# Kernel optimization log

Hardware: AMD Instinct MI355X
Metric: run time of the kernel (lower is better)

The kernel has to match this reference:

```python
import jax, jax.numpy as jnp
import numpy as np

B, T, IN, H, OUT = 4096, 7, 512, 1024, 512


def setup_inputs() -> dict:
    key = jax.random.key(0)
    ks = jax.random.split(key, 13)
    s = 0.05  # weight init scale to keep gates/tanh unsaturated
    return {
        "x": jax.random.normal(ks[0], (B, T, IN), jnp.float32),
        "W_ih1": jax.random.normal(ks[1], (3 * H, IN), jnp.float32) * s,
        "W_hh1": jax.random.normal(ks[2], (3 * H, H), jnp.float32) * s,
        "b_ih1": jax.random.normal(ks[3], (3 * H,), jnp.float32) * s,
        "b_hh1": jax.random.normal(ks[4], (3 * H,), jnp.float32) * s,
        "W_ih2": jax.random.normal(ks[5], (3 * H, H), jnp.float32) * s,
        "W_hh2": jax.random.normal(ks[6], (3 * H, H), jnp.float32) * s,
        "b_ih2": jax.random.normal(ks[7], (3 * H,), jnp.float32) * s,
        "b_hh2": jax.random.normal(ks[8], (3 * H,), jnp.float32) * s,
        "Wo1": jax.random.normal(ks[9], (OUT, H), jnp.float32) * s,
        "bo1": jax.random.normal(ks[10], (OUT,), jnp.float32) * s,
        "Wo2": jax.random.normal(ks[11], (OUT, H), jnp.float32) * s,
        "bo2": jax.random.normal(ks[12], (OUT,), jnp.float32) * s,
    }


def gru_cell(x, h, W_ih, W_hh, b_ih, b_hh):
    # torch.nn.GRUCell math, gate order (r, z, n)
    gi = x @ W_ih.T + b_ih          # [B, 3H]
    gh = h @ W_hh.T + b_hh          # [B, 3H]
    i_r, i_z, i_n = jnp.split(gi, 3, axis=-1)
    h_r, h_z, h_n = jnp.split(gh, 3, axis=-1)
    r = jax.nn.sigmoid(i_r + h_r)
    z = jax.nn.sigmoid(i_z + h_z)
    n = jnp.tanh(i_n + r * h_n)
    return (1.0 - z) * n + z * h


def reference(x, W_ih1, W_hh1, b_ih1, b_hh1, W_ih2, W_hh2, b_ih2, b_hh2,
              Wo1, bo1, Wo2, bo2):
    batch = x.shape[0]
    h1_0 = jnp.zeros((batch, H), x.dtype)
    h2_0 = jnp.zeros((batch, H), x.dtype)

    def step(carry, x_t):
        h1, h2 = carry
        h1 = gru_cell(x_t, h1, W_ih1, W_hh1, b_ih1, b_hh1)
        h2 = gru_cell(h1, h2, W_ih2, W_hh2, b_ih2, b_hh2)
        out = jnp.tanh(h1 @ Wo1.T + bo1) + jnp.tanh(h2 @ Wo2.T + bo2)
        # s_t_cached starts as T zeros and only T steps run, so the popped
        # cached state is always zeros: mse(h2, 0) == mean(h2**2)
        aux = jnp.mean(jnp.square(h2))
        return (h1, h2), (out, aux)

    xs = jnp.swapaxes(x, 0, 1)  # [T, B, IN]
    _, (outs, auxs) = jax.lax.scan(step, (h1_0, h2_0), xs)
    outputs = jnp.swapaxes(outs, 0, 1)  # [B, T, OUT]
    aux_loss = jnp.sum(auxs)
    return outputs, aux_loss
```

## Files before the change

### kernel.cpp

```cpp
#include <hip/hip_runtime.h>
#include <cstdint>

#define BB   4096
#define TT   7
#define INF  512
#define HH   1024
#define OUTF 512
#define G3   3072

typedef short bf16x8 __attribute__((ext_vector_type(8)));
typedef float f32x4  __attribute__((ext_vector_type(4)));

static __device__ __forceinline__ unsigned short f2bf(float f) {
  unsigned u = __float_as_uint(f);
  unsigned r = ((u >> 16) & 1u) + 0x7FFFu;
  return (unsigned short)((u + r) >> 16);
}
static __device__ __forceinline__ float bf2f(unsigned short s) {
  return __uint_as_float(((unsigned)s) << 16);
}

#define GLDS16(gp, lp)                                                        \
  __builtin_amdgcn_global_load_lds(                                           \
      (const __attribute__((address_space(1))) void*)(gp),                    \
      (__attribute__((address_space(3))) void*)(lp), 16, 0, 0)

__device__ __forceinline__ int xcd_swz(int bid, int nwg) {
  return (bid & 7) * (nwg >> 3) + (bid >> 3);
}

__global__ __launch_bounds__(256)
void cvt_f32_to_bf16_x4(const float* __restrict__ in, unsigned short* __restrict__ out, int n4) {
  int i = blockIdx.x * 256 + threadIdx.x;
  if (i >= n4) return;
  const float4 v = ((const float4*)in)[i];
  ushort4 o;
  o.x = f2bf(v.x); o.y = f2bf(v.y); o.z = f2bf(v.z); o.w = f2bf(v.w);
  ((ushort4*)out)[i] = o;
}

template<int BM, int BN, int WM, int WN, int GN>
__device__ __forceinline__ void gemm_core(
    const unsigned short* __restrict__ A, long lda, long bm,
    const unsigned short* __restrict__ Wp, long ldw, int K,
    const float* __restrict__ biasp,
    void* __restrict__ Cp, long ldc,
    const float* __restrict__ addp, long ldadd, int mode)
{
  constexpr int ABUF = BM * 64;
  constexpr int WBUF = BN * 64;
  constexpr int AR = (BM * 8) / 256;
  constexpr int WR = (BN * 8) / 256;
  __shared__ __attribute__((aligned(16))) unsigned short sm[2 * (ABUF + WBUF)];
  unsigned short* As = sm;
  unsigned short* Ws = sm + 2 * ABUF;
  __attribute__((address_space(3))) unsigned short* lAs =
      (__attribute__((address_space(3))) unsigned short*)As;
  __attribute__((address_space(3))) unsigned short* lWs =
      (__attribute__((address_space(3))) unsigned short*)Ws;

  const int tid  = threadIdx.x;
  const int lane = tid & 63;
  const int wid  = tid >> 6;
  const int wr = (wid / GN) * (WM * 16);
  const int wc = (wid % GN) * (WN * 16);
  const int fr = lane & 15;
  const int q2 = lane >> 4;

  const unsigned short* gpa[AR];
  const unsigned short* gpw[WR];
  int lofa[AR], lofw[WR];
#pragma unroll
  for (int r = 0; r < AR; ++r) {
    const int id = r * 256 + tid;
    const int row = id >> 3, cc = id & 7;
    gpa[r] = A + (bm + row) * lda + (cc ^ (row & 7)) * 8;
    lofa[r] = id * 8;
  }
#pragma unroll
  for (int r = 0; r < WR; ++r) {
    const int id = r * 256 + tid;
    const int row = id >> 3, cc = id & 7;
    gpw[r] = Wp + (long)row * ldw + (cc ^ (row & 7)) * 8;
    lofw[r] = id * 8;
  }

#define STAGE(buf, kt) do {                                                   \
    _Pragma("unroll")                                                         \
    for (int r = 0; r < AR; ++r) GLDS16(gpa[r] + (kt), lAs + (buf) * ABUF + lofa[r]); \
    _Pragma("unroll")                                                         \
    for (int r = 0; r < WR; ++r) GLDS16(gpw[r] + (kt), lWs + (buf) * WBUF + lofw[r]); \
  } while (0)

  f32x4 acc[WM][WN] = {};
  STAGE(0, 0);
  __syncthreads();
  const int NK = K >> 6;
  for (int it = 0; it < NK; ++it) {
    const int cur = it & 1;
    if (it + 1 < NK) STAGE(cur ^ 1, (it + 1) << 6);

#pragma unroll
    for (int ks = 0; ks < 2; ++ks) {
      bf16x8 af[WM], wf[WN];
#pragma unroll
      for (int i = 0; i < WM; ++i) {
        const int row = wr + i * 16 + fr;
        const int ch  = (ks * 4 + q2) ^ (row & 7);
        af[i] = *(const bf16x8*)&As[cur * ABUF + row * 64 + ch * 8];
      }
#pragma unroll
      for (int i = 0; i < WN; ++i) {
        const int row = wc + i * 16 + fr;
        const int ch  = (ks * 4 + q2) ^ (row & 7);
        wf[i] = *(const bf16x8*)&Ws[cur * WBUF + row * 64 + ch * 8];
      }
#pragma unroll
      for (int mi = 0; mi < WM; ++mi)
#pragma unroll
        for (int ni = 0; ni < WN; ++ni)
          acc[mi][ni] = __builtin_amdgcn_mfma_f32_16x16x32_bf16(af[mi], wf[ni], acc[mi][ni], 0, 0, 0);
    }
    __syncthreads();
  }
#undef STAGE

  const int q = lane >> 4;
#pragma unroll
  for (int ni = 0; ni < WN; ++ni) {
    const int col = wc + ni * 16 + fr;
    const float bv = biasp[col];
#pragma unroll
    for (int mi = 0; mi < WM; ++mi) {
      const long row = bm + wr + mi * 16 + q * 4;
#pragma unroll
      for (int j = 0; j < 4; ++j) {
        const float v = acc[mi][ni][j] + bv;
        if (mode == 0)      ((float*)Cp)[(row + j) * ldc + col] = v;
        else if (mode == 1) ((float*)Cp)[(row + j) * ldc + col] = tanhf(v);
        else if (mode == 2) ((float*)Cp)[(row + j) * ldc + col] = tanhf(v) + addp[(row + j) * ldadd + col];
        else                ((unsigned short*)Cp)[(row + j) * ldc + col] = f2bf(v);
      }
    }
  }
}

__global__ __launch_bounds__(256)
void k_gi1(const unsigned short* __restrict__ A, long lda,
           const unsigned short* __restrict__ W, const float* __restrict__ bias,
           unsigned short* __restrict__ C, int gx)
{
  const int wg = xcd_swz(blockIdx.x, gridDim.x);
  const int bx = wg % gx, by = wg / gx;
  gemm_core<128,128,4,4,2>(A, lda, (long)bx * 128, W + (long)by * 128 * INF, INF, INF,
                           bias + by * 128, C + by * 128, G3, nullptr, 0, 3);
}

__global__ __launch_bounds__(256)
void k_gh_dual(const unsigned short* __restrict__ h1b, const unsigned short* __restrict__ h2b,
               const unsigned short* __restrict__ W1, const unsigned short* __restrict__ W2,
               const float* __restrict__ b1, const float* __restrict__ b2,
               unsigned short* __restrict__ gh1, unsigned short* __restrict__ gh2)
{
  const int wg = xcd_swz(blockIdx.x, gridDim.x);
  const int bx = wg % 32;
  const int by = (wg / 32) % 24;
  const int z  = wg / (32 * 24);
  const unsigned short* Aa = z ? h2b : h1b;
  const unsigned short* Ww = (z ? W2 : W1) + (long)by * 128 * HH;
  const float* bias = (z ? b2 : b1) + by * 128;
  unsigned short* C = (z ? gh2 : gh1) + by * 128;
  gemm_core<128,128,4,4,2>(Aa, HH, (long)bx * 128, Ww, HH, HH, bias, C, G3, nullptr, 0, 3);
}

__global__ __launch_bounds__(256)
void k_gi2_o1(const unsigned short* __restrict__ h1b,
              const unsigned short* __restrict__ Wih2, const float* __restrict__ bih2,
              unsigned short* __restrict__ gi2,
              const unsigned short* __restrict__ Wo1, const float* __restrict__ bo1,
              float* __restrict__ o1t)
{
  const int wg = xcd_swz(blockIdx.x, gridDim.x);
  const int bx = wg % 32;
  const int by = wg / 32;
  const bool g = (by < 24);
  const int bo = by - 24;
  const unsigned short* Ww = g ? (Wih2 + (long)by * 128 * HH) : (Wo1 + (long)bo * 128 * HH);
  const float* bias        = g ? (bih2 + by * 128)            : (bo1 + bo * 128);
  void* C                  = g ? (void*)(gi2 + by * 128)      : (void*)(o1t + bo * 128);
  const long ldc           = g ? (long)G3 : (long)OUTF;
  gemm_core<128,128,4,4,2>(h1b, HH, (long)bx * 128, Ww, HH, HH, bias, C, ldc,
                           nullptr, 0, g ? 3 : 1);
}

__global__ __launch_bounds__(256)
void k_o2_out(const unsigned short* __restrict__ h2b,
              const unsigned short* __restrict__ Wo2, const float* __restrict__ bo2,
              const float* __restrict__ o1t, float* __restrict__ outp)
{
  const int wg = xcd_swz(blockIdx.x, gridDim.x);
  const int bx = wg % 64;
  const int by = wg / 64;
  gemm_core<64,64,2,2,2>(h2b, HH, (long)bx * 64, Wo2 + (long)by * 64 * HH, HH, HH,
                         bo2 + by * 64, outp + by * 64, (long)TT * OUTF,
                         o1t + by * 64, OUTF, 2);
}

__global__ __launch_bounds__(256)
void k_gate(const unsigned short* __restrict__ gi, long gistride,
            const unsigned short* __restrict__ gh,
            unsigned short* __restrict__ hb,
            float* __restrict__ auxp)
{
  const int i4 = blockIdx.x * 256 + threadIdx.x;
  const int e  = i4 << 2;
  const int b = e >> 10;
  const int c = e & 1023;
  const unsigned short* g = gi + (long)b * gistride + c;
  const ushort4 a0 = *(const ushort4*)(g);
  const ushort4 a1 = *(const ushort4*)(g + HH);
  const ushort4 a2 = *(const ushort4*)(g + 2 * HH);
  const unsigned short* gg = gh + (long)b * G3 + c;
  const ushort4 b0 = *(const ushort4*)(gg);
  const ushort4 b1 = *(const ushort4*)(gg + HH);
  const ushort4 b2 = *(const ushort4*)(gg + 2 * HH);
  const f32x4 ir  = f32x4{bf2f(a0.x), bf2f(a0.y), bf2f(a0.z), bf2f(a0.w)};
  const f32x4 iz  = f32x4{bf2f(a1.x), bf2f(a1.y), bf2f(a1.z), bf2f(a1.w)};
  const f32x4 inn = f32x4{bf2f(a2.x), bf2f(a2.y), bf2f(a2.z), bf2f(a2.w)};
  const f32x4 hr  = f32x4{bf2f(b0.x), bf2f(b0.y), bf2f(b0.z), bf2f(b0.w)};
  const f32x4 hz  = f32x4{bf2f(b1.x), bf2f(b1.y), bf2f(b1.z), bf2f(b1.w)};
  const f32x4 hn  = f32x4{bf2f(b2.x), bf2f(b2.y), bf2f(b2.z), bf2f(b2.w)};
  const ushort4 ho = *(const ushort4*)(hb + e);
  const f32x4 h = f32x4{bf2f(ho.x), bf2f(ho.y), bf2f(ho.z), bf2f(ho.w)};
  f32x4 hnew;
  float vsum = 0.f;
#pragma unroll
  for (int j = 0; j < 4; ++j) {
    const float r = 1.f / (1.f + __expf(-(ir[j] + hr[j])));
    const float z = 1.f / (1.f + __expf(-(iz[j] + hz[j])));
    const float n = tanhf(inn[j] + r * hn[j]);
    hnew[j] = (1.f - z) * n + z * h[j];
    vsum += hnew[j] * hnew[j];
  }
  ushort4 o;
  o.x = f2bf(hnew[0]); o.y = f2bf(hnew[1]); o.z = f2bf(hnew[2]); o.w = f2bf(hnew[3]);
  *(ushort4*)(hb + e) = o;
  if (auxp != nullptr) {
#pragma unroll
    for (int off = 32; off > 0; off >>= 1) vsum += __shfl_down(vsum, off);
    __shared__ float wsum[4];
    if ((threadIdx.x & 63) == 0) wsum[threadIdx.x >> 6] = vsum;
    __syncthreads();
    if (threadIdx.x == 0) auxp[blockIdx.x] = wsum[0] + wsum[1] + wsum[2] + wsum[3];
  }
}

__global__ __launch_bounds__(256)
void aux_reduce(const float* __restrict__ p, int n, float* __restrict__ out, float scale) {
  float s = 0.f;
  for (int i = threadIdx.x; i < n; i += 256) s += p[i];
#pragma unroll
  for (int off = 32; off > 0; off >>= 1) s += __shfl_down(s, off);
  __shared__ float wsum[4];
  if ((threadIdx.x & 63) == 0) wsum[threadIdx.x >> 6] = s;
  __syncthreads();
  if (threadIdx.x == 0) out[0] = (wsum[0] + wsum[1] + wsum[2] + wsum[3]) * scale;
}

extern "C" void kernel_launch(void* const* d_in, const int* in_sizes, int n_in,
                              void* d_out, int out_size, void* d_ws, size_t ws_size,
                              hipStream_t stream) {
  const float* x    = (const float*)d_in[0];
  const float* Wih1 = (const float*)d_in[1];
  const float* Whh1 = (const float*)d_in[2];
  const float* bih1 = (const float*)d_in[3];
  const float* bhh1 = (const float*)d_in[4];
  const float* Wih2 = (const float*)d_in[5];
  const float* Whh2 = (const float*)d_in[6];
  const float* bih2 = (const float*)d_in[7];
  const float* bhh2 = (const float*)d_in[8];
  const float* Wo1  = (const float*)d_in[9];
  const float* bo1  = (const float*)d_in[10];
  const float* Wo2  = (const float*)d_in[11];
  const float* bo2  = (const float*)d_in[12];

  char* ws = (char*)d_ws;
  size_t off = 0;
  auto alloc = [&](size_t bytes) {
    char* p = ws + off;
    off = (off + bytes + 255) & ~(size_t)255;
    return p;
  };

  unsigned short* xb    = (unsigned short*)alloc((size_t)BB * TT * INF * 2);
  unsigned short* wih1b = (unsigned short*)alloc((size_t)G3 * INF * 2);
  unsigned short* whh1b = (unsigned short*)alloc((size_t)G3 * HH * 2);
  unsigned short* wih2b = (unsigned short*)alloc((size_t)G3 * HH * 2);
  unsigned short* whh2b = (unsigned short*)alloc((size_t)G3 * HH * 2);
  unsigned short* wo1b  = (unsigned short*)alloc((size_t)OUTF * HH * 2);
  unsigned short* wo2b  = (unsigned short*)alloc((size_t)OUTF * HH * 2);
  unsigned short* h1b = (unsigned short*)alloc((size_t)BB * HH * 2);
  unsigned short* h2b = (unsigned short*)alloc((size_t)BB * HH * 2);
  unsigned short* gh1 = (unsigned short*)alloc((size_t)BB * G3 * 2);
  unsigned short* gh2 = (unsigned short*)alloc((size_t)BB * G3 * 2);
  float* o1t  = (float*)alloc((size_t)BB * OUTF * 4);
  float* auxp = (float*)alloc((size_t)TT * (BB * HH / 1024) * 4);
  unsigned short* gi2 = gh1;

  const size_t gi1_big   = (size_t)BB * TT * G3 * 2;
  const size_t gi1_small = (size_t)BB * G3 * 2;
  const bool hoist = (off + gi1_big + (size_t)(32 << 20)) <= ws_size;
  unsigned short* gi1b = (unsigned short*)alloc(hoist ? gi1_big : gi1_small);

  float* aux = (float*)d_out + (size_t)BB * TT * OUTF;

  auto cvt = [&](const float* src, unsigned short* dst, size_t n) {
    int n4 = (int)(n / 4);
    cvt_f32_to_bf16_x4<<<dim3((n4 + 255) / 256), dim3(256), 0, stream>>>(src, dst, n4);
  };
  cvt(x,    xb,    (size_t)BB * TT * INF);
  cvt(Wih1, wih1b, (size_t)G3 * INF);
  cvt(Whh1, whh1b, (size_t)G3 * HH);
  cvt(Wih2, wih2b, (size_t)G3 * HH);
  cvt(Whh2, whh2b, (size_t)G3 * HH);
  cvt(Wo1,  wo1b,  (size_t)OUTF * HH);
  cvt(Wo2,  wo2b,  (size_t)OUTF * HH);

  hipMemsetAsync(h1b, 0, (size_t)BB * HH * 2, stream);
  hipMemsetAsync(h2b, 0, (size_t)BB * HH * 2, stream);

  const dim3 blk(256);
  const int gateGrid = BB * HH / 1024;

  if (hoist)
    k_gi1<<<dim3(224 * 24), blk, 0, stream>>>(xb, INF, wih1b, bih1, gi1b, 224);

  for (int t = 0; t < TT; ++t) {
    if (!hoist)
      k_gi1<<<dim3(32 * 24), blk, 0, stream>>>(xb + (size_t)t * INF, (long)TT * INF,
                                               wih1b, bih1, gi1b, 32);
    k_gh_dual<<<dim3(32 * 24 * 2), blk, 0, stream>>>(h1b, h2b, whh1b, whh2b, bhh1, bhh2, gh1, gh2);
    k_gate<<<dim3(gateGrid), blk, 0, stream>>>(
        hoist ? gi1b + (size_t)t * G3 : gi1b, hoist ? (long)TT * G3 : (long)G3,
        gh1, h1b, nullptr);
    k_gi2_o1<<<dim3(32 * 28), blk, 0, stream>>>(h1b, wih2b, bih2, gi2, wo1b, bo1, o1t);
    k_gate<<<dim3(gateGrid), blk, 0, stream>>>(gi2, (long)G3, gh2, h2b,
                                               auxp + (size_t)t * gateGrid);
    k_o2_out<<<dim3(64 * 8), blk, 0, stream>>>(h2b, wo2b, bo2, o1t,
                                               (float*)d_out + (size_t)t * OUTF);
  }
  aux_reduce<<<dim3(1), blk, 0, stream>>>(auxp, TT * gateGrid, aux,
                                          1.f / ((float)BB * (float)HH));
}
```

Measured before the change: 1.416 ms.

## Merge per-step gi1, gh and delayed o2 GEMMs into one launch; single-buffer K=32 tiles

Merges the per-timestep x-projection GEMM, both recurrent hidden GEMMs and the previous step's output-2 GEMM into one grid. This cuts launches and fills the GPU with more workgroups per wave. The hoisted all-timestep input GEMM is dropped in favour of per-step computation. The GEMM core also moves from double-buffered 64-wide K tiles with XOR swizzle to single-buffered 32-wide tiles with no swizzle, halving LDS use. That may raise occupancy, but it adds two barriers per iteration, exposes load latency and risks LDS bank conflicts.

```diff
diff --git a/kernel.cpp b/kernel.cpp
--- a/kernel.cpp
+++ b/kernel.cpp
@@ -47,13 +47,11 @@
     void* __restrict__ Cp, long ldc,
     const float* __restrict__ addp, long ldadd, int mode)
 {
-  constexpr int ABUF = BM * 64;
-  constexpr int WBUF = BN * 64;
-  constexpr int AR = (BM * 8) / 256;
-  constexpr int WR = (BN * 8) / 256;
-  __shared__ __attribute__((aligned(16))) unsigned short sm[2 * (ABUF + WBUF)];
+  constexpr int AR = (BM * 4) / 256;
+  constexpr int WR = (BN * 4) / 256;
+  __shared__ __attribute__((aligned(16))) unsigned short sm[(BM + BN) * 32];
   unsigned short* As = sm;
-  unsigned short* Ws = sm + 2 * ABUF;
+  unsigned short* Ws = sm + BM * 32;
   __attribute__((address_space(3))) unsigned short* lAs =
       (__attribute__((address_space(3))) unsigned short*)As;
   __attribute__((address_space(3))) unsigned short* lWs =
@@ -65,7 +63,7 @@
   const int wr = (wid / GN) * (WM * 16);
   const int wc = (wid % GN) * (WN * 16);
   const int fr = lane & 15;
-  const int q2 = lane >> 4;
+  const int fk = (lane >> 4) * 8;
 
   const unsigned short* gpa[AR];
   const unsigned short* gpw[WR];
@@ -73,57 +71,38 @@
 #pragma unroll
   for (int r = 0; r < AR; ++r) {
     const int id = r * 256 + tid;
-    const int row = id >> 3, cc = id & 7;
-    gpa[r] = A + (bm + row) * lda + (cc ^ (row & 7)) * 8;
+    gpa[r] = A + (bm + (id >> 2)) * lda + (id & 3) * 8;
     lofa[r] = id * 8;
   }
 #pragma unroll
   for (int r = 0; r < WR; ++r) {
     const int id = r * 256 + tid;
-    const int row = id >> 3, cc = id & 7;
-    gpw[r] = Wp + (long)row * ldw + (cc ^ (row & 7)) * 8;
+    gpw[r] = Wp + (long)(id >> 2) * ldw + (id & 3) * 8;
     lofw[r] = id * 8;
   }
 
-#define STAGE(buf, kt) do {                                                   \
-    _Pragma("unroll")                                                         \
-    for (int r = 0; r < AR; ++r) GLDS16(gpa[r] + (kt), lAs + (buf) * ABUF + lofa[r]); \
-    _Pragma("unroll")                                                         \
-    for (int r = 0; r < WR; ++r) GLDS16(gpw[r] + (kt), lWs + (buf) * WBUF + lofw[r]); \
-  } while (0)
-
   f32x4 acc[WM][WN] = {};
-  STAGE(0, 0);
-  __syncthreads();
-  const int NK = K >> 6;
-  for (int it = 0; it < NK; ++it) {
-    const int cur = it & 1;
-    if (it + 1 < NK) STAGE(cur ^ 1, (it + 1) << 6);
-
-#pragma unroll
-    for (int ks = 0; ks < 2; ++ks) {
-      bf16x8 af[WM], wf[WN];
-#pragma unroll
-      for (int i = 0; i < WM; ++i) {
-        const int row = wr + i * 16 + fr;
-        const int ch  = (ks * 4 + q2) ^ (row & 7);
-        af[i] = *(const bf16x8*)&As[cur * ABUF + row * 64 + ch * 8];
-      }
-#pragma unroll
-      for (int i = 0; i < WN; ++i) {
-        const int row = wc + i * 16 + fr;
-        const int ch  = (ks * 4 + q2) ^ (row & 7);
-        wf[i] = *(const bf16x8*)&Ws[cur * WBUF + row * 64 + ch * 8];
-      }
-#pragma unroll
-      for (int mi = 0; mi < WM; ++mi)
-#pragma unroll
-        for (int ni = 0; ni < WN; ++ni)
-          acc[mi][ni] = __builtin_amdgcn_mfma_f32_16x16x32_bf16(af[mi], wf[ni], acc[mi][ni], 0, 0, 0);
-    }
+  for (int kt = 0; kt < K; kt += 32) {
+    if (kt) __syncthreads();
+#pragma unroll
+    for (int r = 0; r < AR; ++r) GLDS16(gpa[r] + kt, lAs + lofa[r]);
+#pragma unroll
+    for (int r = 0; r < WR; ++r) GLDS16(gpw[r] + kt, lWs + lofw[r]);
     __syncthreads();
-  }
-#undef STAGE
+
+    bf16x8 af[WM], wf[WN];
+#pragma unroll
+    for (int i = 0; i < WM; ++i)
+      af[i] = *(const bf16x8*)&As[(wr + i * 16 + fr) * 32 + fk];
+#pragma unroll
+    for (int i = 0; i < WN; ++i)
+      wf[i] = *(const bf16x8*)&Ws[(wc + i * 16 + fr) * 32 + fk];
+#pragma unroll
+    for (int mi = 0; mi < WM; ++mi)
+#pragma unroll
+      for (int ni = 0; ni < WN; ++ni)
+        acc[mi][ni] = __builtin_amdgcn_mfma_f32_16x16x32_bf16(af[mi], wf[ni], acc[mi][ni], 0, 0, 0);
+  }
 
   const int q = lane >> 4;
 #pragma unroll
@@ -146,31 +125,45 @@
 }
 
 __global__ __launch_bounds__(256)
-void k_gi1(const unsigned short* __restrict__ A, long lda,
-           const unsigned short* __restrict__ W, const float* __restrict__ bias,
-           unsigned short* __restrict__ C, int gx)
+void k_step1(const unsigned short* __restrict__ xb_t,
+             const unsigned short* __restrict__ wih1b, const float* __restrict__ bih1,
+             unsigned short* __restrict__ gi1b,
+             const unsigned short* __restrict__ h1b, const unsigned short* __restrict__ h2b,
+             const unsigned short* __restrict__ whh1b, const unsigned short* __restrict__ whh2b,
+             const float* __restrict__ bhh1, const float* __restrict__ bhh2,
+             unsigned short* __restrict__ gh1, unsigned short* __restrict__ gh2,
+             const unsigned short* __restrict__ wo2b, const float* __restrict__ bo2,
+             const float* __restrict__ o1t_prev, float* __restrict__ out_prev)
 {
   const int wg = xcd_swz(blockIdx.x, gridDim.x);
-  const int bx = wg % gx, by = wg / gx;
-  gemm_core<128,128,4,4,2>(A, lda, (long)bx * 128, W + (long)by * 128 * INF, INF, INF,
-                           bias + by * 128, C + by * 128, G3, nullptr, 0, 3);
-}
-
-__global__ __launch_bounds__(256)
-void k_gh_dual(const unsigned short* __restrict__ h1b, const unsigned short* __restrict__ h2b,
-               const unsigned short* __restrict__ W1, const unsigned short* __restrict__ W2,
-               const float* __restrict__ b1, const float* __restrict__ b2,
-               unsigned short* __restrict__ gh1, unsigned short* __restrict__ gh2)
-{
-  const int wg = xcd_swz(blockIdx.x, gridDim.x);
-  const int bx = wg % 32;
-  const int by = (wg / 32) % 24;
-  const int z  = wg / (32 * 24);
-  const unsigned short* Aa = z ? h2b : h1b;
-  const unsigned short* Ww = (z ? W2 : W1) + (long)by * 128 * HH;
-  const float* bias = (z ? b2 : b1) + by * 128;
-  unsigned short* C = (z ? gh2 : gh1) + by * 128;
-  gemm_core<128,128,4,4,2>(Aa, HH, (long)bx * 128, Ww, HH, HH, bias, C, G3, nullptr, 0, 3);
+  const unsigned short* A; long lda; long bm;
+  const unsigned short* W; long ldw; int K;
+  const float* bias; void* C; long ldc; int mode;
+  const float* addp = nullptr; long ldadd = 0;
+  if (wg < 768) {
+    const int bx = wg & 31, by = wg >> 5;
+    A = xb_t; lda = (long)TT * INF; bm = (long)bx * 128;
+    W = wih1b + (long)by * 128 * INF; ldw = INF; K = INF;
+    bias = bih1 + by * 128; C = gi1b + by * 128; ldc = G3; mode = 3;
+  } else if (wg < 2304) {
+    int idx = wg - 768;
+    const int z = idx >= 768;
+    if (z) idx -= 768;
+    const int bx = idx & 31, by = idx >> 5;
+    A = z ? h2b : h1b; lda = HH; bm = (long)bx * 128;
+    W = (z ? whh2b : whh1b) + (long)by * 128 * HH; ldw = HH; K = HH;
+    bias = (z ? bhh2 : bhh1) + by * 128;
+    C = (z ? gh2 : gh1) + by * 128; ldc = G3; mode = 3;
+  } else {
+    const int idx = wg - 2304;
+    const int bx = idx & 31, by = idx >> 5;
+    A = h2b; lda = HH; bm = (long)bx * 128;
+    W = wo2b + (long)by * 128 * HH; ldw = HH; K = HH;
+    bias = bo2 + by * 128;
+    C = out_prev + by * 128; ldc = (long)TT * OUTF; mode = 2;
+    addp = o1t_prev + by * 128; ldadd = OUTF;
+  }
+  gemm_core<128,128,4,4,2>(A, lda, bm, W, ldw, K, bias, C, ldc, addp, ldadd, mode);
 }
 
 __global__ __launch_bounds__(256)
@@ -181,8 +174,8 @@
               float* __restrict__ o1t)
 {
   const int wg = xcd_swz(blockIdx.x, gridDim.x);
-  const int bx = wg % 32;
-  const int by = wg / 32;
+  const int bx = wg & 31;
+  const int by = wg >> 5;
   const bool g = (by < 24);
   const int bo = by - 24;
   const unsigned short* Ww = g ? (Wih2 + (long)by * 128 * HH) : (Wo1 + (long)bo * 128 * HH);
@@ -194,16 +187,16 @@
 }
 
 __global__ __launch_bounds__(256)
-void k_o2_out(const unsigned short* __restrict__ h2b,
-              const unsigned short* __restrict__ Wo2, const float* __restrict__ bo2,
-              const float* __restrict__ o1t, float* __restrict__ outp)
+void k_o2f(const unsigned short* __restrict__ h2b,
+           const unsigned short* __restrict__ Wo2, const float* __restrict__ bo2,
+           const float* __restrict__ o1t, float* __restrict__ outp)
 {
   const int wg = xcd_swz(blockIdx.x, gridDim.x);
-  const int bx = wg % 64;
-  const int by = wg / 64;
-  gemm_core<64,64,2,2,2>(h2b, HH, (long)bx * 64, Wo2 + (long)by * 64 * HH, HH, HH,
-                         bo2 + by * 64, outp + by * 64, (long)TT * OUTF,
-                         o1t + by * 64, OUTF, 2);
+  const int bx = wg & 31;
+  const int by = wg >> 5;
+  gemm_core<128,128,4,4,2>(h2b, HH, (long)bx * 128, Wo2 + (long)by * 128 * HH, HH, HH,
+                           bo2 + by * 128, outp + by * 128, (long)TT * OUTF,
+                           o1t + by * 128, OUTF, 2);
 }
 
 __global__ __launch_bounds__(256)
@@ -303,14 +296,10 @@
   unsigned short* h2b = (unsigned short*)alloc((size_t)BB * HH * 2);
   unsigned short* gh1 = (unsigned short*)alloc((size_t)BB * G3 * 2);
   unsigned short* gh2 = (unsigned short*)alloc((size_t)BB * G3 * 2);
+  unsigned short* gi1b = (unsigned short*)alloc((size_t)BB * G3 * 2);
   float* o1t  = (float*)alloc((size_t)BB * OUTF * 4);
   float* auxp = (float*)alloc((size_t)TT * (BB * HH / 1024) * 4);
   unsigned short* gi2 = gh1;
-
-  const size_t gi1_big   = (size_t)BB * TT * G3 * 2;
-  const size_t gi1_small = (size_t)BB * G3 * 2;
-  const bool hoist = (off + gi1_big + (size_t)(32 << 20)) <= ws_size;
-  unsigned short* gi1b = (unsigned short*)alloc(hoist ? gi1_big : gi1_small);
 
   float* aux = (float*)d_out + (size_t)BB * TT * OUTF;
 
@@ -332,23 +321,19 @@
   const dim3 blk(256);
   const int gateGrid = BB * HH / 1024;
 
-  if (hoist)
-    k_gi1<<<dim3(224 * 24), blk, 0, stream>>>(xb, INF, wih1b, bih1, gi1b, 224);
-
   for (int t = 0; t < TT; ++t) {
-    if (!hoist)
-      k_gi1<<<dim3(32 * 24), blk, 0, stream>>>(xb + (size_t)t * INF, (long)TT * INF,
-                                               wih1b, bih1, gi1b, 32);
-    k_gh_dual<<<dim3(32 * 24 * 2), blk, 0, stream>>>(h1b, h2b, whh1b, whh2b, bhh1, bhh2, gh1, gh2);
-    k_gate<<<dim3(gateGrid), blk, 0, stream>>>(
-        hoist ? gi1b + (size_t)t * G3 : gi1b, hoist ? (long)TT * G3 : (long)G3,
-        gh1, h1b, nullptr);
+    const int d1grid = (t == 0) ? 2304 : 2432;
+    k_step1<<<dim3(d1grid), blk, 0, stream>>>(
+        xb + (size_t)t * INF, wih1b, bih1, gi1b,
+        h1b, h2b, whh1b, whh2b, bhh1, bhh2, gh1, gh2,
+        wo2b, bo2, o1t, (float*)d_out + (size_t)(t > 0 ? t - 1 : 0) * OUTF);
+    k_gate<<<dim3(gateGrid), blk, 0, stream>>>(gi1b, (long)G3, gh1, h1b, nullptr);
     k_gi2_o1<<<dim3(32 * 28), blk, 0, stream>>>(h1b, wih2b, bih2, gi2, wo1b, bo1, o1t);
     k_gate<<<dim3(gateGrid), blk, 0, stream>>>(gi2, (long)G3, gh2, h2b,
                                                auxp + (size_t)t * gateGrid);
-    k_o2_out<<<dim3(64 * 8), blk, 0, stream>>>(h2b, wo2b, bo2, o1t,
-                                               (float*)d_out + (size_t)t * OUTF);
-  }
+  }
+  k_o2f<<<dim3(128), blk, 0, stream>>>(h2b, wo2b, bo2, o1t,
+                                       (float*)d_out + (size_t)(TT - 1) * OUTF);
   aux_reduce<<<dim3(1), blk, 0, stream>>>(auxp, TT * gateGrid, aux,
                                           1.f / ((float)BB * (float)HH));
 }
```

Result: slower. 1.881 ms (+32.8%).

## Use 256x256 tile GEMM with 512-thread blocks and per-step input projection

Applied to the files above, without the earlier changes.

Adds a 256x256-tile GEMM core with 8 waves, each computing 128x64 of the tile, and uses it for the input-projection, hidden-projection and gi2/o1 kernels. This cuts grid sizes to a few hundred workgroups and raises operand reuse per LDS load. The hoisted all-timestep input projection is dropped, so gi1 is now computed each step into a small buffer. The goal is better MFMA density and less LDS and global traffic, at the cost of 128KB of LDS per block, fewer blocks (limited wave-level parallelism), and more register pressure.

```diff
diff --git a/kernel.cpp b/kernel.cpp
--- a/kernel.cpp
+++ b/kernel.cpp
@@ -37,6 +37,122 @@
   ushort4 o;
   o.x = f2bf(v.x); o.y = f2bf(v.y); o.z = f2bf(v.z); o.w = f2bf(v.w);
   ((ushort4*)out)[i] = o;
+}
+
+__device__ __forceinline__ void gemm256_core(
+    const unsigned short* __restrict__ A, long lda, long bm,
+    const unsigned short* __restrict__ Wp, long ldw, int K,
+    const float* __restrict__ biasp,
+    void* __restrict__ Cp, long ldc,
+    const float* __restrict__ addp, long ldadd, int mode)
+{
+  constexpr int TBUF = 256 * 64;
+  __shared__ __attribute__((aligned(16))) unsigned short sm[4 * TBUF];
+  unsigned short* As = sm;
+  unsigned short* Ws = sm + 2 * TBUF;
+  __attribute__((address_space(3))) unsigned short* lAs =
+      (__attribute__((address_space(3))) unsigned short*)As;
+  __attribute__((address_space(3))) unsigned short* lWs =
+      (__attribute__((address_space(3))) unsigned short*)Ws;
+
+  const int tid  = threadIdx.x;
+  const int lane = tid & 63;
+  const int wid  = tid >> 6;
+  const int wr = (wid >> 2) * 128;
+  const int wc = (wid & 3) * 64;
+  const int fr = lane & 15;
+  const int q2 = lane >> 4;
+
+  const unsigned short* gpa[4];
+  const unsigned short* gpw[4];
+  int lof[4];
+#pragma unroll
+  for (int r = 0; r < 4; ++r) {
+    const int id = r * 512 + tid;
+    const int row = id >> 3, cc = id & 7;
+    gpa[r] = A + (bm + row) * lda + (cc ^ (row & 7)) * 8;
+    gpw[r] = Wp + (long)row * ldw + (cc ^ (row & 7)) * 8;
+    lof[r] = id * 8;
+  }
+
+#define STAGE256(buf, kt) do {                                                \
+    _Pragma("unroll")                                                         \
+    for (int r = 0; r < 4; ++r) GLDS16(gpa[r] + (kt), lAs + (buf) * TBUF + lof[r]); \
+    _Pragma("unroll")                                                         \
+    for (int r = 0; r < 4; ++r) GLDS16(gpw[r] + (kt), lWs + (buf) * TBUF + lof[r]); \
+  } while (0)
+
+  f32x4 acc[8][4] = {};
+  STAGE256(0, 0);
+  __syncthreads();
+  const int NT = K >> 6;
+  for (int it = 0; it < NT; ++it) {
+    const int cur = it & 1;
+    if (it + 1 < NT) STAGE256(cur ^ 1, (it + 1) << 6);
+
+    bf16x8 bfr[4][2];
+#pragma unroll
+    for (int ni = 0; ni < 4; ++ni)
+#pragma unroll
+      for (int ks = 0; ks < 2; ++ks) {
+        const int row = wc + ni * 16 + fr;
+        const int ch  = (ks * 4 + q2) ^ (row & 7);
+        bfr[ni][ks] = *(const bf16x8*)&Ws[cur * TBUF + row * 64 + ch * 8];
+      }
+    {
+      bf16x8 af[8];
+#pragma unroll
+      for (int mi = 0; mi < 8; ++mi) {
+        const int row = wr + mi * 16 + fr;
+        const int ch  = q2 ^ (row & 7);
+        af[mi] = *(const bf16x8*)&As[cur * TBUF + row * 64 + ch * 8];
+      }
+      __builtin_amdgcn_s_setprio(1);
+#pragma unroll
+      for (int mi = 0; mi < 8; ++mi)
+#pragma unroll
+        for (int ni = 0; ni < 4; ++ni)
+          acc[mi][ni] = __builtin_amdgcn_mfma_f32_16x16x32_bf16(af[mi], bfr[ni][0], acc[mi][ni], 0, 0, 0);
+      __builtin_amdgcn_s_setprio(0);
+    }
+    {
+      bf16x8 af[8];
+#pragma unroll
+      for (int mi = 0; mi < 8; ++mi) {
+        const int row = wr + mi * 16 + fr;
+        const int ch  = (4 + q2) ^ (row & 7);
+        af[mi] = *(const bf16x8*)&As[cur * TBUF + row * 64 + ch * 8];
+      }
+      __builtin_amdgcn_s_setprio(1);
+#pragma unroll
+      for (int mi = 0; mi < 8; ++mi)
+#pragma unroll
+        for (int ni = 0; ni < 4; ++ni)
+          acc[mi][ni] = __builtin_amdgcn_mfma_f32_16x16x32_bf16(af[mi], bfr[ni][1], acc[mi][ni], 0, 0, 0);
+      __builtin_amdgcn_s_setprio(0);
+    }
+    __syncthreads();
+  }
+#undef STAGE256
+
+  const int q = lane >> 4;
+#pragma unroll
+  for (int ni = 0; ni < 4; ++ni) {
+    const int col = wc + ni * 16 + fr;
+    const float bv = biasp[col];
+#pragma unroll
+    for (int mi = 0; mi < 8; ++mi) {
+      const long row = bm + wr + mi * 16 + q * 4;
+#pragma unroll
+      for (int j = 0; j < 4; ++j) {
+        const float v = acc[mi][ni][j] + bv;
+        if (mode == 0)      ((float*)Cp)[(row + j) * ldc + col] = v;
+        else if (mode == 1) ((float*)Cp)[(row + j) * ldc + col] = tanhf(v);
+        else if (mode == 2) ((float*)Cp)[(row + j) * ldc + col] = tanhf(v) + addp[(row + j) * ldadd + col];
+        else                ((unsigned short*)Cp)[(row + j) * ldc + col] = f2bf(v);
+      }
+    }
+  }
 }
 
 template<int BM, int BN, int WM, int WN, int GN>
@@ -99,7 +215,6 @@
   for (int it = 0; it < NK; ++it) {
     const int cur = it & 1;
     if (it + 1 < NK) STAGE(cur ^ 1, (it + 1) << 6);
-
 #pragma unroll
     for (int ks = 0; ks < 2; ++ks) {
       bf16x8 af[WM], wf[WN];
@@ -145,35 +260,36 @@
   }
 }
 
-__global__ __launch_bounds__(256)
-void k_gi1(const unsigned short* __restrict__ A, long lda,
+__global__ __launch_bounds__(512, 2)
+void k_gi1(const unsigned short* __restrict__ A,
            const unsigned short* __restrict__ W, const float* __restrict__ bias,
-           unsigned short* __restrict__ C, int gx)
+           unsigned short* __restrict__ C)
 {
   const int wg = xcd_swz(blockIdx.x, gridDim.x);
-  const int bx = wg % gx, by = wg / gx;
-  gemm_core<128,128,4,4,2>(A, lda, (long)bx * 128, W + (long)by * 128 * INF, INF, INF,
-                           bias + by * 128, C + by * 128, G3, nullptr, 0, 3);
-}
-
-__global__ __launch_bounds__(256)
+  const int bx = wg & 15, by = wg >> 4;
+  gemm256_core(A, (long)TT * INF, (long)bx * 256, W + (long)by * 256 * INF, INF, INF,
+               bias + by * 256, C + by * 256, G3, nullptr, 0, 3);
+}
+
+__global__ __launch_bounds__(512, 2)
 void k_gh_dual(const unsigned short* __restrict__ h1b, const unsigned short* __restrict__ h2b,
                const unsigned short* __restrict__ W1, const unsigned short* __restrict__ W2,
                const float* __restrict__ b1, const float* __restrict__ b2,
                unsigned short* __restrict__ gh1, unsigned short* __restrict__ gh2)
 {
   const int wg = xcd_swz(blockIdx.x, gridDim.x);
-  const int bx = wg % 32;
-  const int by = (wg / 32) % 24;
-  const int z  = wg / (32 * 24);
+  const int bx = wg & 15;
+  const int r  = wg >> 4;
+  const int z  = r >= 12;
+  const int by = z ? r - 12 : r;
   const unsigned short* Aa = z ? h2b : h1b;
-  const unsigned short* Ww = (z ? W2 : W1) + (long)by * 128 * HH;
-  const float* bias = (z ? b2 : b1) + by * 128;
-  unsigned short* C = (z ? gh2 : gh1) + by * 128;
-  gemm_core<128,128,4,4,2>(Aa, HH, (long)bx * 128, Ww, HH, HH, bias, C, G3, nullptr, 0, 3);
-}
-
-__global__ __launch_bounds__(256)
+  const unsigned short* Ww = (z ? W2 : W1) + (long)by * 256 * HH;
+  const float* bias = (z ? b2 : b1) + by * 256;
+  unsigned short* C = (z ? gh2 : gh1) + by * 256;
+  gemm256_core(Aa, HH, (long)bx * 256, Ww, HH, HH, bias, C, G3, nullptr, 0, 3);
+}
+
+__global__ __launch_bounds__(512, 2)
 void k_gi2_o1(const unsigned short* __restrict__ h1b,
               const unsigned short* __restrict__ Wih2, const float* __restrict__ bih2,
               unsigned short* __restrict__ gi2,
@@ -181,16 +297,16 @@
               float* __restrict__ o1t)
 {
   const int wg = xcd_swz(blockIdx.x, gridDim.x);
-  const int bx = wg % 32;
-  const int by = wg / 32;
-  const bool g = (by < 24);
-  const int bo = by - 24;
-  const unsigned short* Ww = g ? (Wih2 + (long)by * 128 * HH) : (Wo1 + (long)bo * 128 * HH);
-  const float* bias        = g ? (bih2 + by * 128)            : (bo1 + bo * 128);
-  void* C                  = g ? (void*)(gi2 + by * 128)      : (void*)(o1t + bo * 128);
+  const bool g = (wg < 192);
+  const int idx = g ? wg : wg - 192;
+  const int bx = idx & 15;
+  const int by = idx >> 4;
+  const unsigned short* Ww = g ? (Wih2 + (long)by * 256 * HH) : (Wo1 + (long)by * 256 * HH);
+  const float* bias        = g ? (bih2 + by * 256)            : (bo1 + by * 256);
+  void* C                  = g ? (void*)(gi2 + by * 256)      : (void*)(o1t + by * 256);
   const long ldc           = g ? (long)G3 : (long)OUTF;
-  gemm_core<128,128,4,4,2>(h1b, HH, (long)bx * 128, Ww, HH, HH, bias, C, ldc,
-                           nullptr, 0, g ? 3 : 1);
+  gemm256_core(h1b, HH, (long)bx * 256, Ww, HH, HH, bias, C, ldc,
+               nullptr, 0, g ? 3 : 1);
 }
 
 __global__ __launch_bounds__(256)
@@ -303,14 +419,10 @@
   unsigned short* h2b = (unsigned short*)alloc((size_t)BB * HH * 2);
   unsigned short* gh1 = (unsigned short*)alloc((size_t)BB * G3 * 2);
   unsigned short* gh2 = (unsigned short*)alloc((size_t)BB * G3 * 2);
+  unsigned short* gi1b = (unsigned short*)alloc((size_t)BB * G3 * 2);
   float* o1t  = (float*)alloc((size_t)BB * OUTF * 4);
   float* auxp = (float*)alloc((size_t)TT * (BB * HH / 1024) * 4);
   unsigned short* gi2 = gh1;
-
-  const size_t gi1_big   = (size_t)BB * TT * G3 * 2;
-  const size_t gi1_small = (size_t)BB * G3 * 2;
-  const bool hoist = (off + gi1_big + (size_t)(32 << 20)) <= ws_size;
-  unsigned short* gi1b = (unsigned short*)alloc(hoist ? gi1_big : gi1_small);
 
   float* aux = (float*)d_out + (size_t)BB * TT * OUTF;
 
@@ -330,24 +442,18 @@
   hipMemsetAsync(h2b, 0, (size_t)BB * HH * 2, stream);
 
   const dim3 blk(256);
+  const dim3 blk512(512);
   const int gateGrid = BB * HH / 1024;
 
-  if (hoist)
-    k_gi1<<<dim3(224 * 24), blk, 0, stream>>>(xb, INF, wih1b, bih1, gi1b, 224);
-
   for (int t = 0; t < TT; ++t) {
-    if (!hoist)
-      k_gi1<<<dim3(32 * 24), blk, 0, stream>>>(xb + (size_t)t * INF, (long)TT * INF,
-                                               wih1b, bih1, gi1b, 32);
-    k_gh_dual<<<dim3(32 * 24 * 2), blk, 0, stream>>>(h1b, h2b, whh1b, whh2b, bhh1, bhh2, gh1, gh2);
-    k_gate<<<dim3(gateGrid), blk, 0, stream>>>(
-        hoist ? gi1b + (size_t)t * G3 : gi1b, hoist ? (long)TT * G3 : (long)G3,
-        gh1, h1b, nullptr);
-    k_gi2_o1<<<dim3(32 * 28), blk, 0, stream>>>(h1b, wih2b, bih2, gi2, wo1b, bo1, o1t);
+    k_gi1<<<dim3(192), blk512, 0, stream>>>(xb + (size_t)t * INF, wih1b, bih1, gi1b);
+    k_gh_dual<<<dim3(384), blk512, 0, stream>>>(h1b, h2b, whh1b, whh2b, bhh1, bhh2, gh1, gh2);
+    k_gate<<<dim3(gateGrid), blk, 0, stream>>>(gi1b, (long)G3, gh1, h1b, nullptr);
+    k_gi2_o1<<<dim3(224), blk512, 0, stream>>>(h1b, wih2b, bih2, gi2, wo1b, bo1, o1t);
     k_gate<<<dim3(gateGrid), blk, 0, stream>>>(gi2, (long)G3, gh2, h2b,
                                                auxp + (size_t)t * gateGrid);
-    k_o2_out<<<dim3(64 * 8), blk, 0, stream>>>(h2b, wo2b, bo2, o1t,
-                                               (float*)d_out + (size_t)t * OUTF);
+    k_o2_out<<<dim3(512), blk, 0, stream>>>(h2b, wo2b, bo2, o1t,
+                                            (float*)d_out + (size_t)t * OUTF);
   }
   aux_reduce<<<dim3(1), blk, 0, stream>>>(auxp, TT * gateGrid, aux,
                                           1.f / ((float)BB * (float)HH));
```

New measurement: 1.660 ms. 17.2% more time.
